# Optimization experiments

Hardware: AMD Instinct MI355X
Metric: run time of the kernel (lower is better)

## Reference

```python
import jax, jax.numpy as jnp
import numpy as np

# DilationSumLayer with kernel_size=(7,7), padding='same' (pad=3 per side).
# The torch module's unfold (dense L @ x @ R matmuls) + kron(ones, weight) add
# + MaxPool2d(7, stride=7) is exactly grayscale morphological dilation:
#   out[..., i, j] = max_{a,b} ( xpad[..., i+a, j+b] + w[a, b] )
KH, KW = 7, 7
PAD = 3  # kernel_size // 2, 'same' padding, zero-padded (F.pad default)


def setup_inputs() -> dict:
    key = jax.random.key(0)
    k1, k2 = jax.random.split(key)
    x = jax.random.normal(k1, (8, 8, 512, 512), dtype=jnp.float32)      # (B, C, H, W)
    weight = jax.random.normal(k2, (KH, KW), dtype=jnp.float32)          # structuring element
    return {"x": x, "weight": weight}


def reference(x, weight):
    kh, kw = KH, KW
    xp = jnp.pad(x, ((0, 0), (0, 0), (PAD, PAD), (PAD, PAD)))  # (B, C, H+2p, W+2p)
    Ho = xp.shape[-2] - kh + 1  # == H ('same')
    Wo = xp.shape[-1] - kw + 1  # == W
    # Running max over the 49 fixed kernel offsets (small static loop; each
    # iteration is a fused shifted-view add + elementwise max, no big stack).
    out = jnp.full(x.shape[:-2] + (Ho, Wo), -jnp.inf, dtype=x.dtype)
    for a in range(kh):
        for b in range(kw):
            out = jnp.maximum(out, xp[..., a:a + Ho, b:b + Wo] + weight[a, b])
    return out
```

## Files before the change

kernel.cpp:

```cpp
#include <hip/hip_runtime.h>


#define HH 512
#define WW 512

typedef float v2f __attribute__((ext_vector_type(2)));

__device__ __align__(16) const float ZP4[4] = {0.f, 0.f, 0.f, 0.f};

__device__ __forceinline__ float max3f(float a, float b, float c) {
  float d;
  asm("v_max3_f32 %0, %1, %2, %3" : "=v"(d) : "v"(a), "v"(b), "v"(c));
  return d;
}

#define ONEOUT(T, K, J, P1, P2, P3, S)                                       \
  {                                                                          \
    const int a_ = (K) - (T);                                                \
    const v2f c01_ = (P1) + w2[a_][0];                     \
    const v2f c23_ = (P2) + w2[a_][1];                                       \
    const v2f c45_ = (P3) + w2[a_][2];                                       \
    const float c6_ = (S) + w6[a_];                                          \
    const float t1_ = max3f(c01_.x, c01_.y, c23_.x);                         \
    const float t2_ = max3f(c23_.y, c45_.x, c45_.y);                         \
    acc[T][J] = ((K) == (T))                                                 \
                    ? max3f(t1_, t2_, c6_)                  \
                    : max3f(t1_, t2_, fmaxf(c6_, acc[T][J]));                \
  }

#define COMPROW(E, K)                                                        \
  {                                                                          \
    const v2f o0_ = (v2f){E[0].y, E[1].x};                                   \
    const v2f o1_ = (v2f){E[1].y, E[2].x};                                   \
    const v2f o2_ = (v2f){E[2].y, E[3].x};                                   \
    const v2f o3_ = (v2f){E[3].y, E[4].x};                                   \
    _Pragma("unroll") for (int t = 0; t < 4; ++t) {                          \
      if (t <= (K) && t + 6 >= (K)) {                                        \
        ONEOUT(t, K, 0, o0_, o1_, o2_, E[3].y);                              \
        ONEOUT(t, K, 1, E[1], E[2], E[3], E[4].x);                           \
        ONEOUT(t, K, 2, o1_, o2_, o3_, E[4].y);                              \
        ONEOUT(t, K, 3, E[2], E[3], E[4], E[5].x);                           \
      }                                                                      \
    }                                                                        \
  }

#define LOADDS(E, K)                                                         \
  {                                                                          \
    int o_ = bando + tr4 + (K);                                              \
    o_ -= (o_ >= 38) ? 38 : 0;                                               \
    const float* lr_ = ldsf + o_ * 264 + lc4;                                \
    float4 v0_ = *reinterpret_cast<const float4*>(lr_);                      \
    float4 v1_ = *reinterpret_cast<const float4*>(lr_ + 4);                  \
    float4 v2_ = *reinterpret_cast<const float4*>(lr_ + 8);                  \
    E[0] = (v2f){v0_.x, v0_.y};  E[1] = (v2f){v0_.z, v0_.w};                 \
    E[2] = (v2f){v1_.x, v1_.y};  E[3] = (v2f){v1_.z, v1_.w};                 \
    E[4] = (v2f){v2_.x, v2_.y};  E[5] = (v2f){v2_.z, v2_.w};                 \
  }

#define STOREROW4(T)                                                         \
  {                                                                          \
    float* orow_ = op + (ptrdiff_t)(rowband + tr4 + (T)) * WW + col0;        \
    *reinterpret_cast<float4*>(orow_) =                                      \
        make_float4(acc[T][0], acc[T][1], acc[T][2], acc[T][3]);             \
  }

__global__ __launch_bounds__(256) void dilate7(const float* __restrict__ x,
                                               const float* __restrict__ wg,
                                               float* __restrict__ out) {
  __shared__ float ldsf[38 * 264];

  const int tid = threadIdx.x;
  const int lc = tid & 63;
  const int lc4 = lc << 2;
  const int colbase = blockIdx.x * 256;
  const int col0 = colbase + lc4;
  const int tr4 = __builtin_amdgcn_readfirstlane((tid >> 6) << 2);
  const int row0blk = blockIdx.y * 64;

  const size_t plane_off = (size_t)blockIdx.z * (size_t)(HH * WW);
  const float* xp = x + plane_off;
  float* op = out + plane_off;

  float wv[49];
#pragma unroll
  for (int i = 0; i < 49; ++i)
    wv[i] = __int_as_float(__builtin_amdgcn_readfirstlane(__float_as_int(wg[i])));
  v2f w2[7][3];
  float w6[7];
#pragma unroll
  for (int a = 0; a < 7; ++a) {
    w2[a][0] = (v2f){wv[7 * a + 0], wv[7 * a + 1]};
    w2[a][1] = (v2f){wv[7 * a + 2], wv[7 * a + 3]};
    w2[a][2] = (v2f){wv[7 * a + 4], wv[7 * a + 5]};
    w6[a] = wv[7 * a + 6];
  }

  {
    unsigned r_ = __umulhi((unsigned)tid, 0x7C1F07C4u) >> 5;
    int c_ = tid - (int)r_ * 66;
#pragma unroll
    for (int i = 0; i < 6; ++i) {
      int q = i * 256 + tid;
      if (q < 1452) {
        int g = row0blk - 3 + (int)r_;
        int gc = colbase - 4 + (c_ << 2);
        bool ok = ((unsigned)g < (unsigned)HH) && ((unsigned)gc < (unsigned)WW);
        const float* src = ok ? (xp + (ptrdiff_t)g * WW + gc) : &ZP4[0];
        float4 v = *reinterpret_cast<const float4*>(src);
        *reinterpret_cast<float4*>(ldsf + (int)r_ * 264 + (c_ << 2)) = v;
      }
      r_ += 3; c_ += 58; if (c_ >= 66) { c_ -= 66; ++r_; }
    }
  }
  __syncthreads();

  float acc[4][4];
  v2f rvA[6], rvB[6];

#pragma unroll 1
  for (int b = 0; b < 4; ++b) {
    const int bando = 16 * b;
    const int rowband = row0blk + bando;

    float4 sv[5];
    if (b < 3) {
      unsigned r_ = __umulhi((unsigned)tid, 0x7C1F07C4u) >> 5;
      int c_ = tid - (int)r_ * 66;
      const int grb = row0blk + bando + 19;
#pragma unroll
      for (int i = 0; i < 5; ++i) {
        if (i < 4 || tid < 32) {
          int g = grb + (int)r_;
          int gc = colbase - 4 + (c_ << 2);
          bool ok = ((unsigned)g < (unsigned)HH) && ((unsigned)gc < (unsigned)WW);
          const float* src = ok ? (xp + (ptrdiff_t)g * WW + gc) : &ZP4[0];
          sv[i] = *reinterpret_cast<const float4*>(src);
        }
        r_ += 3; c_ += 58; if (c_ >= 66) { c_ -= 66; ++r_; }
      }
    }

    LOADDS(rvA, 0);
    LOADDS(rvB, 1);  COMPROW(rvA, 0);
    LOADDS(rvA, 2);  COMPROW(rvB, 1);
    LOADDS(rvB, 3);  COMPROW(rvA, 2);
    LOADDS(rvA, 4);  COMPROW(rvB, 3);
    LOADDS(rvB, 5);  COMPROW(rvA, 4);
    LOADDS(rvA, 6);  COMPROW(rvB, 5);
    LOADDS(rvB, 7);  COMPROW(rvA, 6);  STOREROW4(0);
    LOADDS(rvA, 8);  COMPROW(rvB, 7);  STOREROW4(1);
    LOADDS(rvB, 9);  COMPROW(rvA, 8);  STOREROW4(2);
                     COMPROW(rvB, 9);  STOREROW4(3);

    if (b < 3) {
      unsigned r_ = __umulhi((unsigned)tid, 0x7C1F07C4u) >> 5;
      int c_ = tid - (int)r_ * 66;
      int sb = bando + 22; sb -= (sb >= 38) ? 38 : 0;
#pragma unroll
      for (int i = 0; i < 5; ++i) {
        if (i < 4 || tid < 32) {
          *reinterpret_cast<float4*>(ldsf + (sb + (int)r_) * 264 + (c_ << 2)) = sv[i];
        }
        r_ += 3; c_ += 58; if (c_ >= 66) { c_ -= 66; ++r_; }
      }
      __syncthreads();
    }
  }
}

extern "C" void kernel_launch(void* const* d_in, const int* in_sizes, int n_in,
                              void* d_out, int out_size, void* d_ws, size_t ws_size,
                              hipStream_t stream) {
  const float* x = (const float*)d_in[0];
  const float* w = (const float*)d_in[1];
  float* out = (float*)d_out;
  const int planes = in_sizes[0] / (HH * WW);
  dim3 grid(2, 8, planes);
  dilate7<<<grid, dim3(256, 1, 1), 0, stream>>>(x, w, out);
}
```

Baseline: 49.42 us.

## Stage input tiles into LDS with direct global-to-LDS async loads

Replaces the register-staged global loads and later LDS stores with global_load_lds 16-byte direct-to-LDS transfers, for both the initial halo tile and the per-band prefetch into the ring buffer. This is meant to remove the register round trip and VGPR pressure from the prefetch so the loads overlap the compute of the current band. The address mapping relies on lane-contiguous LDS destinations (wave base plus lane times 16 bytes), and the loop now always syncs at the end, including the last band. Correctness depends on the implicit waitcnt before the barrier covering the async LDS writes.

```diff
diff --git a/kernel.cpp b/kernel.cpp
--- a/kernel.cpp
+++ b/kernel.cpp
@@ -13,6 +13,32 @@
   asm("v_max3_f32 %0, %1, %2, %3" : "=v"(d) : "v"(a), "v"(b), "v"(c));
   return d;
 }
+
+__device__ __forceinline__ void gl_lds16(const float* g, void* l) {
+  __builtin_amdgcn_global_load_lds(
+      (const __attribute__((address_space(1))) void*)g,
+      (__attribute__((address_space(3))) void*)l, 16, 0, 0);
+}
+
+#define STAGE(SLOT, GRB, NC)                                                 \
+  {                                                                          \
+    unsigned r_ = __umulhi((unsigned)tid, 0x7C1F07C4u) >> 5;     \
+    int c_ = tid - (int)r_ * 66;                                             \
+    _Pragma("unroll") for (int i_ = 0; i_ < ((NC) + 255) / 256; ++i_) {      \
+      int q_ = i_ * 256 + tid;                                               \
+      if (q_ < (NC)) {                                                       \
+        int g_ = (GRB) + (int)r_;                                            \
+        int gc_ = colbase - 4 + (c_ << 2);                                   \
+        bool ok_ = ((unsigned)g_ < (unsigned)HH) &&                          \
+                   ((unsigned)gc_ < (unsigned)WW);                           \
+        const float* src_ = ok_ ? (xp + (ptrdiff_t)g_ * WW + gc_) : &ZP4[0]; \
+        void* dst_ =                                                         \
+            (void*)((char*)(ring + (SLOT) * 66) + ((i_ * 256 + w64) << 4));  \
+        gl_lds16(src_, dst_);                                                \
+      }                                                                      \
+      r_ += 3; c_ += 58; if (c_ >= 66) { c_ -= 66; ++r_; }     \
+    }                                                                        \
+  }
 
 #define ONEOUT(T, K, J, P1, P2, P3, S)                                       \
   {                                                                          \
@@ -48,10 +74,10 @@
   {                                                                          \
     int o_ = bando + tr4 + (K);                                              \
     o_ -= (o_ >= 38) ? 38 : 0;                                               \
-    const float* lr_ = ldsf + o_ * 264 + lc4;                                \
-    float4 v0_ = *reinterpret_cast<const float4*>(lr_);                      \
-    float4 v1_ = *reinterpret_cast<const float4*>(lr_ + 4);                  \
-    float4 v2_ = *reinterpret_cast<const float4*>(lr_ + 8);                  \
+    const float4* lr_ = ring + o_ * 66 + lc;                                 \
+    float4 v0_ = lr_[0];                                                     \
+    float4 v1_ = lr_[1];                                                     \
+    float4 v2_ = lr_[2];                                                     \
     E[0] = (v2f){v0_.x, v0_.y};  E[1] = (v2f){v0_.z, v0_.w};                 \
     E[2] = (v2f){v1_.x, v1_.y};  E[3] = (v2f){v1_.z, v1_.w};                 \
     E[4] = (v2f){v2_.x, v2_.y};  E[5] = (v2f){v2_.z, v2_.w};                 \
@@ -67,14 +93,14 @@
 __global__ __launch_bounds__(256) void dilate7(const float* __restrict__ x,
                                                const float* __restrict__ wg,
                                                float* __restrict__ out) {
-  __shared__ float ldsf[38 * 264];
+  __shared__ float4 ring[38 * 66];
 
   const int tid = threadIdx.x;
   const int lc = tid & 63;
-  const int lc4 = lc << 2;
   const int colbase = blockIdx.x * 256;
-  const int col0 = colbase + lc4;
+  const int col0 = colbase + (lc << 2);
   const int tr4 = __builtin_amdgcn_readfirstlane((tid >> 6) << 2);
+  const int w64 = __builtin_amdgcn_readfirstlane((tid >> 6) << 6);
   const int row0blk = blockIdx.y * 64;
 
   const size_t plane_off = (size_t)blockIdx.z * (size_t)(HH * WW);
@@ -95,23 +121,7 @@
     w6[a] = wv[7 * a + 6];
   }
 
-  {
-    unsigned r_ = __umulhi((unsigned)tid, 0x7C1F07C4u) >> 5;
-    int c_ = tid - (int)r_ * 66;
-#pragma unroll
-    for (int i = 0; i < 6; ++i) {
-      int q = i * 256 + tid;
-      if (q < 1452) {
-        int g = row0blk - 3 + (int)r_;
-        int gc = colbase - 4 + (c_ << 2);
-        bool ok = ((unsigned)g < (unsigned)HH) && ((unsigned)gc < (unsigned)WW);
-        const float* src = ok ? (xp + (ptrdiff_t)g * WW + gc) : &ZP4[0];
-        float4 v = *reinterpret_cast<const float4*>(src);
-        *reinterpret_cast<float4*>(ldsf + (int)r_ * 264 + (c_ << 2)) = v;
-      }
-      r_ += 3; c_ += 58; if (c_ >= 66) { c_ -= 66; ++r_; }
-    }
-  }
+  STAGE(0, row0blk - 3, 1452);
   __syncthreads();
 
   float acc[4][4];
@@ -122,22 +132,10 @@
     const int bando = 16 * b;
     const int rowband = row0blk + bando;
 
-    float4 sv[5];
     if (b < 3) {
-      unsigned r_ = __umulhi((unsigned)tid, 0x7C1F07C4u) >> 5;
-      int c_ = tid - (int)r_ * 66;
-      const int grb = row0blk + bando + 19;
-#pragma unroll
-      for (int i = 0; i < 5; ++i) {
-        if (i < 4 || tid < 32) {
-          int g = grb + (int)r_;
-          int gc = colbase - 4 + (c_ << 2);
-          bool ok = ((unsigned)g < (unsigned)HH) && ((unsigned)gc < (unsigned)WW);
-          const float* src = ok ? (xp + (ptrdiff_t)g * WW + gc) : &ZP4[0];
-          sv[i] = *reinterpret_cast<const float4*>(src);
-        }
-        r_ += 3; c_ += 58; if (c_ >= 66) { c_ -= 66; ++r_; }
-      }
+      int sb = bando + 22;
+      sb -= (sb >= 38) ? 38 : 0;
+      STAGE(sb, rowband + 19, 1056);
     }
 
     LOADDS(rvA, 0);
@@ -152,19 +150,7 @@
     LOADDS(rvB, 9);  COMPROW(rvA, 8);  STOREROW4(2);
                      COMPROW(rvB, 9);  STOREROW4(3);
 
-    if (b < 3) {
-      unsigned r_ = __umulhi((unsigned)tid, 0x7C1F07C4u) >> 5;
-      int c_ = tid - (int)r_ * 66;
-      int sb = bando + 22; sb -= (sb >= 38) ? 38 : 0;
-#pragma unroll
-      for (int i = 0; i < 5; ++i) {
-        if (i < 4 || tid < 32) {
-          *reinterpret_cast<float4*>(ldsf + (sb + (int)r_) * 264 + (c_ << 2)) = sv[i];
-        }
-        r_ += 3; c_ += 58; if (c_ >= 66) { c_ -= 66; ++r_; }
-      }
-      __syncthreads();
-    }
+    __syncthreads();
   }
 }
 
```

After: 46.63 us. 1.06x faster.
